# Kernel optimization log

Measured on AMD Instinct MI355X. Metric: run time of the kernel, lower is better.

The kernel has to match this reference:

```python
import jax, jax.numpy as jnp
import numpy as np
import math

D = 768
H = 12
HD = D // H  # 64


def setup_inputs() -> dict:
    key = jax.random.key(0)
    ks = jax.random.split(key, 8)
    B, S = 32, 127
    desc = jax.random.normal(ks[0], (B, S, D), dtype=jnp.float32)
    nv = jax.random.normal(ks[1], (B, S + 1, D), dtype=jnp.float32)
    def xavier(k, shape):
        fan_in, fan_out = shape[1], shape[0]
        gain = 1.0 / math.sqrt(2.0)
        limit = gain * math.sqrt(6.0 / (fan_in + fan_out))
        return jax.random.uniform(k, shape, jnp.float32, -limit, limit)
    Wq = xavier(ks[2], (D, D)); bq = jnp.zeros((D,), jnp.float32)
    Wk = xavier(ks[3], (D, D)); bk = jnp.zeros((D,), jnp.float32)
    Wv = xavier(ks[4], (D, D)); bv = jnp.zeros((D,), jnp.float32)
    # attn_proj: Linear(3*head_dim, 1)
    Wa = xavier(ks[5], (1, 3 * HD))[0]  # [3*HD]
    ba = jnp.zeros((), jnp.float32)
    return {
        "desc_embeddings": desc,
        "name_value_embeddings": nv,
        "Wq": Wq, "bq": bq, "Wk": Wk, "bk": bk, "Wv": Wv, "bv": bv,
        "Wa": Wa, "ba": ba,
    }


def _forward(desc_embeddings, name_value_embeddings, Wq, bq, Wk, bk, Wv, bv, Wa, ba):
    B, new_seq, _ = name_value_embeddings.shape
    S = new_seq - 1

    # adjacency: var-var all ones, CLS->Var row = 1, Var->CLS col = 0, CLS->CLS = 0
    adj = jnp.zeros((new_seq, new_seq), jnp.float32)
    adj = adj.at[1:, 1:].set(1.0)
    adj = adj.at[0, 1:].set(1.0)
    adj = jnp.broadcast_to(adj, (B, new_seq, new_seq))

    # q,k,v: [B, H, new_seq, HD]
    def proj(W, b):
        y = name_value_embeddings @ W.T + b
        return y.reshape(B, new_seq, H, HD).transpose(0, 2, 1, 3)
    q = proj(Wq, bq); k = proj(Wk, bk); v = proj(Wv, bv)

    # attn_proj weight split: [q_part | k_part | edge_part], each [HD]
    wq_a, wk_a, we_a = Wa[:HD], Wa[HD:2 * HD], Wa[2 * HD:]

    # q/k scalar contributions per (b,h,i) and (b,h,j)
    lq = jnp.einsum('bhid,d->bhi', q, wq_a)  # [B,H,new_seq]
    lk = jnp.einsum('bhjd,d->bhj', k, wk_a)  # [B,H,new_seq]

    # edge_attr[b,i,j] per head h (head slice of concat[node_i_desc, node_j_desc]):
    # edge vector = concat(desc_i, desc_j)[h*HD:(h+1)*HD] viewed as [H, HD] of 2D dims.
    # concat(desc_i, desc_j) has 2D dims -> reshaped to [H, HD] means head h takes
    # slice [h*HD:(h+1)*HD] of the 2D-dim concat. Heads 0..H/2-1 come from desc_i,
    # heads H/2..H-1 come from desc_j. Compute edge dot with we_a accordingly.
    # desc_full[b,t] : [B,S,D]. Build per-head contributions:
    # for h < H//2: edge slice = desc_i[h*HD:(h+1)*HD]  -> depends only on i
    # for h >= H//2: edge slice = desc_j[(h-H//2)*HD:(h-H//2+1)*HD] -> depends only on j
    desc_heads = desc_embeddings.reshape(B, S, H // 2, 2 * HD)  # wrong split; do directly
    # Direct: per head h, slice indices into the 2D concat vector
    dh = desc_embeddings.reshape(B, S, H, HD)  # desc split into H chunks of HD (covers D = H*HD)
    # concat(desc_i,desc_j) reshaped to [H,HD]: heads 0..H/2-1 use dh_i[:, :, h],
    # heads H/2..H-1 use dh_j[:, :, h - H/2]
    e_dot = jnp.einsum('bshd,d->bsh', dh, jnp.broadcast_to(we_a, (HD,)))  # placeholder, recompute per head below
    # per-head edge scalar contribution for var-var edges:
    ei = jnp.einsum('bshd,d->bhs', dh, we_a)  # contribution if head slice comes from desc at position s
    Hh = H // 2
    # var-var logits edge part: for h<Hh depends on i; for h>=Hh depends on j
    le_i = ei[:, :Hh, :]   # [B,Hh,S] depends on i (row)
    le_j = ei[:, Hh:, :]   # [B,Hh,S] depends on j (col)

    # CLS edges: cls_edge_attr = concat(desc, desc) at position t (the var index)
    # row 0 (CLS->var j): edge = concat(desc_j, desc_j) -> head h slice:
    #   h<Hh: dh_j[h]; h>=Hh: dh_j[h-Hh]  -> scalar ei[b,h,j] with h mapped
    e_cls = jnp.concatenate([ei[:, :Hh, :], ei[:, :Hh, :]], axis=1) * 0  # init
    e_cls = jnp.concatenate([le_i, le_i], axis=1)  # [B,H,S]: head h<Hh uses dh[h], h>=Hh uses dh[h-Hh]
    # note ei[:, :Hh] corresponds to dh chunks 0..Hh-1 ; for h>=Hh slice is dh[h-Hh] -> same le_i

    # Assemble full logits [B,H,new_seq,new_seq]
    logits = lq[:, :, :, None] + lk[:, :, None, :]
    # edge contributions (only where adj==1; edge_attr zeroed elsewhere by mask mult)
    edge = jnp.zeros((B, H, new_seq, new_seq), jnp.float32)
    # var-var block [1:,1:]
    ev = jnp.zeros((B, H, S, S), jnp.float32)
    ev = ev + jnp.pad(le_i, ((0, 0), (0, Hh), (0, 0)))[:, :, :, None] * 0  # keep shapes
    ev_i = jnp.concatenate([le_i, jnp.zeros_like(le_j)], axis=1)  # h<Hh: i-dependent
    ev_j = jnp.concatenate([jnp.zeros_like(le_i), le_j], axis=1)  # h>=Hh: j-dependent
    ev = ev_i[:, :, :, None] + ev_j[:, :, None, :]  # [B,H,S,S]
    edge = edge.at[:, :, 1:, 1:].set(ev)
    # CLS row (0, 1:): cls_edge = concat(desc_j,desc_j); j = column var
    edge = edge.at[:, :, 0, 1:].set(e_cls)
    # CLS col (1:, 0): cls_edge = concat(desc_i,desc_i) BUT adj[:,1:,0]=0 so edge_attr
    # multiplied by adj -> zero; also masked out. edge stays 0, but torch zeroes it too.
    # mask edge by adjacency (edge_attr *= adj)
    edge = edge * adj[:, None, :, :]
    logits = logits + edge + ba

    mask = (adj[:, None, :, :] == 0).astype(jnp.float32) * -1e9
    logits = logits + mask
    attn = jax.nn.softmax(logits, axis=-1)  # [B,H,new_seq,new_seq]
    ctx = jnp.einsum('bhij,bhjd->bhid', attn, v)
    basis_outputs = ctx.transpose(0, 2, 1, 3)  # [B,new_seq,H,HD]
    return basis_outputs, attn


def reference(desc_embeddings, name_value_embeddings, Wq, bq, Wk, bk, Wv, bv, Wa, ba):
    return _forward(desc_embeddings, name_value_embeddings, Wq, bq, Wk, bk, Wv, bv, Wa, ba)
```

## Files before the change

kernel.cpp:

```cpp
#include <hip/hip_runtime.h>

#define NB 32
#define NS 128
#define SD 127
#define ND 768
#define NH 12
#define HD 64

__device__ inline float wredSum(float v){
  #pragma unroll
  for (int off=32; off>0; off>>=1) v += __shfl_xor(v, off);
  return v;
}
__device__ inline float wredMax(float v){
  #pragma unroll
  for (int off=32; off>0; off>>=1) v = fmaxf(v, __shfl_xor(v, off));
  return v;
}

__global__ __launch_bounds__(256)
void fold_ei(const float* __restrict__ Wk, const float* __restrict__ bk,
             const float* __restrict__ desc, const float* __restrict__ Wa,
             float* __restrict__ uk, float* __restrict__ bkdot,
             float* __restrict__ ei){
  int blk = blockIdx.x, t = threadIdx.x;
  int wave = t >> 6, lane = t & 63;
  if (blk < 144){
    __shared__ float red[4][64];
    int h = blk/12, cb = blk%12;
    int c0 = t & 63, dg = t >> 6;
    const float* base = Wk + (size_t)(h*HD + dg*16)*ND + cb*64 + c0;
    float acc = 0.f;
    #pragma unroll
    for (int i=0;i<16;++i) acc += base[(size_t)i*ND] * Wa[64 + dg*16 + i];
    red[dg][c0] = acc;
    __syncthreads();
    if (dg==0) uk[h*ND + cb*64 + c0] = red[0][c0]+red[1][c0]+red[2][c0]+red[3][c0];
    if (blk==0 && t < NH){
      float a = 0.f;
      for (int d=0; d<64; ++d) a += bk[t*HD+d]*Wa[64+d];
      bkdot[t] = a;
    }
  } else {
    int bs = blk - 144;
    int b = bs / SD, s = bs % SD;
    float wea = Wa[128 + lane];
    const float* row = desc + (size_t)bs * ND;
    #pragma unroll
    for (int hh=0; hh<3; ++hh){
      int h = wave + hh*4;
      float v = row[h*HD + lane] * wea;
      v = wredSum(v);
      if (lane==0) ei[(size_t)(b*NH + h)*NS + s] = v;
    }
  }
}

__global__ __launch_bounds__(256)
void lk_kernel(const float* __restrict__ nv, const float* __restrict__ uk,
               const float* __restrict__ bkdot, float* __restrict__ lk){
  __shared__ __align__(16) float S[4*ND];
  int blk = blockIdx.x, t = threadIdx.x, wave = t>>6, lane = t&63;
  float ukr[3][12], bkd[3];
  #pragma unroll
  for (int hh=0; hh<3; ++hh){
    int h = wave*3 + hh;
    bkd[hh] = bkdot[h];
    #pragma unroll
    for (int k=0;k<12;++k) ukr[hh][k] = uk[h*ND + lane + 64*k];
  }
  int j0 = blk*4;
  const float4* src = (const float4*)(nv + (size_t)j0*ND);
  ((float4*)S)[t]     = src[t];
  ((float4*)S)[t+256] = src[t+256];
  ((float4*)S)[t+512] = src[t+512];
  __syncthreads();
  float acc[12];
  #pragma unroll
  for (int rr=0; rr<4; ++rr)
    #pragma unroll
    for (int hh=0; hh<3; ++hh){
      float a = 0.f;
      #pragma unroll
      for (int k=0;k<12;++k) a += S[rr*ND + lane + 64*k]*ukr[hh][k];
      acc[rr*3+hh] = a;
    }
  #pragma unroll
  for (int i=0;i<12;++i) acc[i] = wredSum(acc[i]);
  if (lane == 0){
    int b = j0 >> 7, jb = j0 & 127;
    #pragma unroll
    for (int rr=0; rr<4; ++rr)
      #pragma unroll
      for (int hh=0; hh<3; ++hh)
        lk[(size_t)(b*NH + wave*3 + hh)*NS + jb + rr] = acc[rr*3+hh] + bkd[hh];
  }
}

__global__ __launch_bounds__(256)
void attn_fused(const float* __restrict__ nv, const float* __restrict__ lk,
                const float* __restrict__ ei, const float* __restrict__ Wv,
                const float* __restrict__ bv, float* __restrict__ out){
  int logical = ((blockIdx.x & 7) * 48) + (blockIdx.x >> 3);
  int b = logical / NH, h = logical % NH;
  int t = threadIdx.x, wave = t >> 6, lane = t & 63;
  __shared__ __align__(16) float slk[NS];
  __shared__ __align__(16) float sei0[NS];
  __shared__ __align__(16) float sei1[NS];
  __shared__ __align__(16) float wf0[NS];
  __shared__ __align__(16) float wf1[NS];
  __shared__ __align__(16) float msum0[ND];
  __shared__ __align__(16) float msum1[ND];
  __shared__ __align__(16) float cvec0[HD];
  __shared__ __align__(16) float cvec1[HD];

  if (t < NS) slk[t] = lk[(size_t)(b*NH + h)*NS + t];
  if (t < SD) sei0[t] = ei[(size_t)(b*NH + (h % 6))*NS + t];
  if (t >= 128 && t < 128 + SD) sei1[t-128] = ei[(size_t)(b*NH + h)*NS + (t-128)];
  __syncthreads();

  if (wave < 2){
    const float* eir = (wave==0) ? sei0 : sei1;
    float g = (wave==0) ? 1.f : (h >= 6 ? 1.f : 0.f);
    float x0 = (lane>=1) ? slk[lane] + g*eir[lane-1] : -3.0e38f;
    float x1 = slk[lane+64] + g*eir[lane+63];
    float mm = wredMax(fmaxf(x0,x1));
    float e0 = (lane>=1) ? __expf(x0-mm) : 0.f;
    float e1 = __expf(x1-mm);
    float s  = wredSum(e0+e1);
    float inv = 1.f/s;
    float* wf = (wave==0) ? wf0 : wf1;
    wf[lane]    = e0*inv;
    wf[lane+64] = e1*inv;
  }
  __syncthreads();

  if (wave < 3){
    const float4* nvb = (const float4*)(nv + (size_t)b*NS*ND);
    float4 a0 = make_float4(0.f,0.f,0.f,0.f);
    float4 a1 = make_float4(0.f,0.f,0.f,0.f);
    #pragma unroll 4
    for (int j=1; j<NS; ++j){
      float4 x = nvb[(size_t)j*192 + t];
      float w0 = wf0[j], w1 = wf1[j];
      a0.x += w0*x.x; a0.y += w0*x.y; a0.z += w0*x.z; a0.w += w0*x.w;
      a1.x += w1*x.x; a1.y += w1*x.y; a1.z += w1*x.z; a1.w += w1*x.w;
    }
    ((float4*)msum0)[t] = a0;
    ((float4*)msum1)[t] = a1;
  } else {
    float4* abase = (float4*)(out + (size_t)NB*NS*ND + (size_t)(b*NH + h)*NS*NS);
    const float4* w0v = (const float4*)wf0;
    const float4* w1v = (const float4*)wf1;
    #pragma unroll
    for (int k=0; k<64; ++k){
      int idx = lane + k*64;
      int q = idx & 31;
      abase[idx] = (idx < 32) ? w0v[q] : w1v[q];
    }
  }
  __syncthreads();

  const float* wvh = Wv + (size_t)h*HD*ND;
  #pragma unroll
  for (int dd=0; dd<16; ++dd){
    int d = wave*16 + dd;
    const float* wvr = wvh + (size_t)d*ND;
    float p0=0.f, p1=0.f;
    #pragma unroll
    for (int k=0; k<12; ++k){
      float wv = wvr[lane + 64*k];
      p0 += wv*msum0[lane + 64*k];
      p1 += wv*msum1[lane + 64*k];
    }
    p0 = wredSum(p0); p1 = wredSum(p1);
    if (lane==0){
      float bb = bv[h*HD + d];
      cvec0[d] = p0 + bb;
      cvec1[d] = p1 + bb;
    }
  }
  __syncthreads();

  float* bo = out + (size_t)b*NS*ND + h*HD;
  const float4* c0 = (const float4*)cvec0;
  const float4* c1 = (const float4*)cvec1;
  #pragma unroll
  for (int k=0; k<8; ++k){
    int idx = t + k*256;
    int i = idx >> 4, q = idx & 15;
    *(float4*)(bo + (size_t)i*ND + q*4) = (i==0) ? c0[q] : c1[q];
  }
}

extern "C" void kernel_launch(void* const* d_in, const int* in_sizes, int n_in,
                              void* d_out, int out_size, void* d_ws, size_t ws_size,
                              hipStream_t stream) {
  const float* desc = (const float*)d_in[0];
  const float* nv   = (const float*)d_in[1];
  const float* Wk   = (const float*)d_in[4];
  const float* bk   = (const float*)d_in[5];
  const float* Wv   = (const float*)d_in[6];
  const float* bv   = (const float*)d_in[7];
  const float* Wa   = (const float*)d_in[8];
  float* out = (float*)d_out;
  float* ws  = (float*)d_ws;

  float* uk     = ws;
  float* bkdot  = ws + 9216;
  float* eibuf  = ws + 9232;
  float* lkbuf  = ws + 58384;

  fold_ei   <<<4208, 256, 0, stream>>>(Wk, bk, desc, Wa, uk, bkdot, eibuf);
  lk_kernel <<<1024, 256, 0, stream>>>(nv, uk, bkdot, lkbuf);
  attn_fused<<<384,  256, 0, stream>>>(nv, lkbuf, eibuf, Wv, bv, out);
}
```

Before: 136.8 us.

## Split attention value reduction across all waves and merge ei into lk kernel

The weighted sum over nv rows in attn_fused is now split over all four waves, each handling 32 rows across three float4 columns. Partial results go to shared memory and are reduced afterwards, and all waves share the attention-matrix store. The per-row edge dot products (ei) move out of the Wk fold kernel into the lk kernel as extra blocks, using float4 loads and 16-lane shuffle reductions, so the first kernel shrinks to 144 blocks. This trades more shared memory (about 24 KB of partials) and one extra barrier for more parallelism and memory-level concurrency in the nv streaming loop.

```diff
diff --git a/kernel.cpp b/kernel.cpp
--- a/kernel.cpp
+++ b/kernel.cpp
@@ -19,81 +19,91 @@
 }
 
 __global__ __launch_bounds__(256)
-void fold_ei(const float* __restrict__ Wk, const float* __restrict__ bk,
-             const float* __restrict__ desc, const float* __restrict__ Wa,
-             float* __restrict__ uk, float* __restrict__ bkdot,
-             float* __restrict__ ei){
+void fold_uk(const float* __restrict__ Wk, const float* __restrict__ bk,
+             const float* __restrict__ Wa, float* __restrict__ uk,
+             float* __restrict__ bkdot){
   int blk = blockIdx.x, t = threadIdx.x;
-  int wave = t >> 6, lane = t & 63;
-  if (blk < 144){
-    __shared__ float red[4][64];
-    int h = blk/12, cb = blk%12;
-    int c0 = t & 63, dg = t >> 6;
-    const float* base = Wk + (size_t)(h*HD + dg*16)*ND + cb*64 + c0;
-    float acc = 0.f;
-    #pragma unroll
-    for (int i=0;i<16;++i) acc += base[(size_t)i*ND] * Wa[64 + dg*16 + i];
-    red[dg][c0] = acc;
+  __shared__ float red[4][64];
+  int h = blk/12, cb = blk%12;
+  int c0 = t & 63, dg = t >> 6;
+  const float* base = Wk + (size_t)(h*HD + dg*16)*ND + cb*64 + c0;
+  float acc = 0.f;
+  #pragma unroll
+  for (int i=0;i<16;++i) acc += base[(size_t)i*ND] * Wa[64 + dg*16 + i];
+  red[dg][c0] = acc;
+  __syncthreads();
+  if (dg==0) uk[h*ND + cb*64 + c0] = red[0][c0]+red[1][c0]+red[2][c0]+red[3][c0];
+  if (blk==0 && t < NH){
+    float a = 0.f;
+    for (int d=0; d<64; ++d) a += bk[t*HD+d]*Wa[64+d];
+    bkdot[t] = a;
+  }
+}
+
+__global__ __launch_bounds__(256)
+void lk_ei(const float* __restrict__ nv, const float* __restrict__ uk,
+           const float* __restrict__ bkdot, const float* __restrict__ Wa,
+           const float* __restrict__ desc, float* __restrict__ lk,
+           float* __restrict__ ei){
+  int blk = blockIdx.x, t = threadIdx.x, wave = t>>6, lane = t&63;
+  if (blk < 1024){
+    __shared__ __align__(16) float S[4*ND];
+    float ukr[3][12], bkd[3];
+    #pragma unroll
+    for (int hh=0; hh<3; ++hh){
+      int h = wave*3 + hh;
+      bkd[hh] = bkdot[h];
+      #pragma unroll
+      for (int k=0;k<12;++k) ukr[hh][k] = uk[h*ND + lane + 64*k];
+    }
+    int j0 = blk*4;
+    const float4* src = (const float4*)(nv + (size_t)j0*ND);
+    ((float4*)S)[t]     = src[t];
+    ((float4*)S)[t+256] = src[t+256];
+    ((float4*)S)[t+512] = src[t+512];
     __syncthreads();
-    if (dg==0) uk[h*ND + cb*64 + c0] = red[0][c0]+red[1][c0]+red[2][c0]+red[3][c0];
-    if (blk==0 && t < NH){
-      float a = 0.f;
-      for (int d=0; d<64; ++d) a += bk[t*HD+d]*Wa[64+d];
-      bkdot[t] = a;
+    float acc[12];
+    #pragma unroll
+    for (int rr=0; rr<4; ++rr)
+      #pragma unroll
+      for (int hh=0; hh<3; ++hh){
+        float a = 0.f;
+        #pragma unroll
+        for (int k=0;k<12;++k) a += S[rr*ND + lane + 64*k]*ukr[hh][k];
+        acc[rr*3+hh] = a;
+      }
+    #pragma unroll
+    for (int i=0;i<12;++i) acc[i] = wredSum(acc[i]);
+    if (lane == 0){
+      int b = j0 >> 7, jb = j0 & 127;
+      #pragma unroll
+      for (int rr=0; rr<4; ++rr)
+        #pragma unroll
+        for (int hh=0; hh<3; ++hh)
+          lk[(size_t)(b*NH + wave*3 + hh)*NS + jb + rr] = acc[rr*3+hh] + bkd[hh];
     }
   } else {
-    int bs = blk - 144;
+    int bs = (blk - 1024)*4 + wave;
     int b = bs / SD, s = bs % SD;
-    float wea = Wa[128 + lane];
-    const float* row = desc + (size_t)bs * ND;
-    #pragma unroll
-    for (int hh=0; hh<3; ++hh){
-      int h = wave + hh*4;
-      float v = row[h*HD + lane] * wea;
-      v = wredSum(v);
-      if (lane==0) ei[(size_t)(b*NH + h)*NS + s] = v;
-    }
-  }
-}
-
-__global__ __launch_bounds__(256)
-void lk_kernel(const float* __restrict__ nv, const float* __restrict__ uk,
-               const float* __restrict__ bkdot, float* __restrict__ lk){
-  __shared__ __align__(16) float S[4*ND];
-  int blk = blockIdx.x, t = threadIdx.x, wave = t>>6, lane = t&63;
-  float ukr[3][12], bkd[3];
-  #pragma unroll
-  for (int hh=0; hh<3; ++hh){
-    int h = wave*3 + hh;
-    bkd[hh] = bkdot[h];
-    #pragma unroll
-    for (int k=0;k<12;++k) ukr[hh][k] = uk[h*ND + lane + 64*k];
-  }
-  int j0 = blk*4;
-  const float4* src = (const float4*)(nv + (size_t)j0*ND);
-  ((float4*)S)[t]     = src[t];
-  ((float4*)S)[t+256] = src[t+256];
-  ((float4*)S)[t+512] = src[t+512];
-  __syncthreads();
-  float acc[12];
-  #pragma unroll
-  for (int rr=0; rr<4; ++rr)
-    #pragma unroll
-    for (int hh=0; hh<3; ++hh){
-      float a = 0.f;
-      #pragma unroll
-      for (int k=0;k<12;++k) a += S[rr*ND + lane + 64*k]*ukr[hh][k];
-      acc[rr*3+hh] = a;
-    }
-  #pragma unroll
-  for (int i=0;i<12;++i) acc[i] = wredSum(acc[i]);
-  if (lane == 0){
-    int b = j0 >> 7, jb = j0 & 127;
-    #pragma unroll
-    for (int rr=0; rr<4; ++rr)
-      #pragma unroll
-      for (int hh=0; hh<3; ++hh)
-        lk[(size_t)(b*NH + wave*3 + hh)*NS + jb + rr] = acc[rr*3+hh] + bkd[hh];
+    const float4* row = (const float4*)(desc + (size_t)bs*ND);
+    float4 r0 = row[lane], r1 = row[lane+64], r2 = row[lane+128];
+    float4 wa4 = ((const float4*)(Wa + 128))[lane & 15];
+    float p0 = r0.x*wa4.x + r0.y*wa4.y + r0.z*wa4.z + r0.w*wa4.w;
+    float p1 = r1.x*wa4.x + r1.y*wa4.y + r1.z*wa4.z + r1.w*wa4.w;
+    float p2 = r2.x*wa4.x + r2.y*wa4.y + r2.z*wa4.z + r2.w*wa4.w;
+    #pragma unroll
+    for (int off=1; off<16; off<<=1){
+      p0 += __shfl_xor(p0, off);
+      p1 += __shfl_xor(p1, off);
+      p2 += __shfl_xor(p2, off);
+    }
+    if ((lane & 15) == 0){
+      int hb = lane >> 4;
+      float* er = ei + (size_t)b*NH*NS + s;
+      er[(size_t)(hb    )*NS] = p0;
+      er[(size_t)(hb + 4)*NS] = p1;
+      er[(size_t)(hb + 8)*NS] = p2;
+    }
   }
 }
 
@@ -104,15 +114,16 @@
   int logical = ((blockIdx.x & 7) * 48) + (blockIdx.x >> 3);
   int b = logical / NH, h = logical % NH;
   int t = threadIdx.x, wave = t >> 6, lane = t & 63;
-  __shared__ __align__(16) float slk[NS];
-  __shared__ __align__(16) float sei0[NS];
-  __shared__ __align__(16) float sei1[NS];
+  __shared__ float slk[NS];
+  __shared__ float sei0[NS];
+  __shared__ float sei1[NS];
   __shared__ __align__(16) float wf0[NS];
   __shared__ __align__(16) float wf1[NS];
+  __shared__ __align__(16) float part[4][2][ND];
   __shared__ __align__(16) float msum0[ND];
   __shared__ __align__(16) float msum1[ND];
-  __shared__ __align__(16) float cvec0[HD];
-  __shared__ __align__(16) float cvec1[HD];
+  __shared__ float cvec0[HD];
+  __shared__ float cvec1[HD];
 
   if (t < NS) slk[t] = lk[(size_t)(b*NH + h)*NS + t];
   if (t < SD) sei0[t] = ei[(size_t)(b*NH + (h % 6))*NS + t];
@@ -135,29 +146,57 @@
   }
   __syncthreads();
 
-  if (wave < 3){
-    const float4* nvb = (const float4*)(nv + (size_t)b*NS*ND);
-    float4 a0 = make_float4(0.f,0.f,0.f,0.f);
-    float4 a1 = make_float4(0.f,0.f,0.f,0.f);
+  {
+    const float4* nvb = (const float4*)(nv + (size_t)b*NS*ND)
+                      + (size_t)(wave*32)*192;
+    float4 a0[3], a1[3];
+    #pragma unroll
+    for (int c=0;c<3;++c){
+      a0[c] = make_float4(0.f,0.f,0.f,0.f);
+      a1[c] = make_float4(0.f,0.f,0.f,0.f);
+    }
     #pragma unroll 4
-    for (int j=1; j<NS; ++j){
-      float4 x = nvb[(size_t)j*192 + t];
-      float w0 = wf0[j], w1 = wf1[j];
-      a0.x += w0*x.x; a0.y += w0*x.y; a0.z += w0*x.z; a0.w += w0*x.w;
-      a1.x += w1*x.x; a1.y += w1*x.y; a1.z += w1*x.z; a1.w += w1*x.w;
-    }
-    ((float4*)msum0)[t] = a0;
-    ((float4*)msum1)[t] = a1;
-  } else {
+    for (int jj=0; jj<32; ++jj){
+      float w0 = wf0[wave*32 + jj], w1 = wf1[wave*32 + jj];
+      #pragma unroll
+      for (int c=0;c<3;++c){
+        float4 x = nvb[(size_t)jj*192 + lane + 64*c];
+        a0[c].x += w0*x.x; a0[c].y += w0*x.y; a0[c].z += w0*x.z; a0[c].w += w0*x.w;
+        a1[c].x += w1*x.x; a1[c].y += w1*x.y; a1[c].z += w1*x.z; a1[c].w += w1*x.w;
+      }
+    }
+    #pragma unroll
+    for (int c=0;c<3;++c){
+      ((float4*)part[wave][0])[lane + 64*c] = a0[c];
+      ((float4*)part[wave][1])[lane + 64*c] = a1[c];
+    }
+  }
+
+  {
     float4* abase = (float4*)(out + (size_t)NB*NS*ND + (size_t)(b*NH + h)*NS*NS);
     const float4* w0v = (const float4*)wf0;
     const float4* w1v = (const float4*)wf1;
     #pragma unroll
-    for (int k=0; k<64; ++k){
-      int idx = lane + k*64;
+    for (int k=0; k<16; ++k){
+      int idx = t + k*256;
       int q = idx & 31;
       abase[idx] = (idx < 32) ? w0v[q] : w1v[q];
     }
+  }
+  __syncthreads();
+
+  if (t < 192){
+    float4 s0 = make_float4(0.f,0.f,0.f,0.f);
+    float4 s1 = make_float4(0.f,0.f,0.f,0.f);
+    #pragma unroll
+    for (int w=0; w<4; ++w){
+      float4 v0 = ((const float4*)part[w][0])[t];
+      float4 v1 = ((const float4*)part[w][1])[t];
+      s0.x += v0.x; s0.y += v0.y; s0.z += v0.z; s0.w += v0.w;
+      s1.x += v1.x; s1.y += v1.y; s1.z += v1.z; s1.w += v1.w;
+    }
+    ((float4*)msum0)[t] = s0;
+    ((float4*)msum1)[t] = s1;
   }
   __syncthreads();
 
@@ -211,7 +250,7 @@
   float* eibuf  = ws + 9232;
   float* lkbuf  = ws + 58384;
 
-  fold_ei   <<<4208, 256, 0, stream>>>(Wk, bk, desc, Wa, uk, bkdot, eibuf);
-  lk_kernel <<<1024, 256, 0, stream>>>(nv, uk, bkdot, lkbuf);
+  fold_uk   <<<144,  256, 0, stream>>>(Wk, bk, Wa, uk, bkdot);
+  lk_ei     <<<2040, 256, 0, stream>>>(nv, uk, bkdot, Wa, desc, lkbuf, eibuf);
   attn_fused<<<384,  256, 0, stream>>>(nv, lkbuf, eibuf, Wv, bv, out);
 }
```

After: 127.2 us. 1.08x faster.
